# Kernel tuning notes

Hardware: AMD Instinct MI355X
Metric: run time of the kernel (lower is better)

## Reference

```python
import jax, jax.numpy as jnp
import numpy as np
from jax import lax

IN_CH = 256
FILTERS_PER_CH = 2            # expansion = 1 -> 2 filters per input channel
INTER_CH = IN_CH * FILTERS_PER_CH
BUTTERFLY_SIZE = 8
BUTTERFLIES = INTER_CH // 2 // BUTTERFLY_SIZE  # 32
WING = BUTTERFLY_SIZE // 2                      # 4


def setup_inputs() -> dict:
    key = jax.random.key(0)
    k1, k2 = jax.random.split(key)
    x = jax.random.normal(k1, (32, IN_CH, 56, 56), dtype=jnp.float32)
    # depthwise conv weight, PyTorch OIHW with groups=IN_CH: (INTER_CH, 1, 3, 3)
    w = jax.random.normal(k2, (INTER_CH, 1, 3, 3), dtype=jnp.float32) * 0.1
    return {"x": x, "w": w}


def reference(x, w):
    # grouped (depthwise, channel multiplier 2) conv, stride 1, pad 1, no bias
    y = lax.conv_general_dilated(
        x, w,
        window_strides=(1, 1),
        padding=[(1, 1), (1, 1)],
        feature_group_count=IN_CH,
        dimension_numbers=("NCHW", "OIHW", "NCHW"),
    )  # (B, INTER_CH, H, W); channels group-major: 2i,2i+1 from input i
    B, C2, H, W = y.shape
    # extract_sequences: consecutive channels alternate between the two outputs
    y = y.reshape(B, C2 // 2, 2, H, W)
    x1 = y[:, :, 0]  # (B, IN_CH, H, W)
    x2 = y[:, :, 1]
    # swap_wings: within each butterfly, swap the two wings
    s = x2.reshape(B, BUTTERFLIES, 2, WING, H, W)
    x2 = jnp.flip(s, axis=2).reshape(B, C2 // 2, H, W)
    return x1 + x2
```

## Files before the change

### kernel.cpp

```cpp
#include <hip/hip_runtime.h>

#define IN_CH 256
#define IMG_H 56
#define IMG_W 56

typedef float v4f __attribute__((ext_vector_type(4)));

__global__ __launch_bounds__(256) void dwconv_butterfly(
    const float* __restrict__ x, const float* __restrict__ wgt,
    float* __restrict__ out)
{
    const int tid = threadIdx.x;
    const int s   = tid >> 4;
    const int i   = tid & 15;
    const bool active = (s < 14) && (i < 14);

    const int p  = blockIdx.x;
    const int b  = blockIdx.y;
    const int c0 = ((p >> 2) << 3) | (p & 3);
    const int c1 = c0 ^ 4;

    const size_t chan = (size_t)IMG_H * IMG_W;
    const float* x0 = x + ((size_t)b * IN_CH + c0) * chan;
    const float* x1 = x + ((size_t)b * IN_CH + c1) * chan;
    float* o0 = out + ((size_t)b * IN_CH + c0) * chan;
    float* o1 = out + ((size_t)b * IN_CH + c1) * chan;

    float wa[9], wb[9], wc[9], wd[9];
    {
        const float* pa = wgt + (size_t)(2 * c0) * 9;
        const float* pb = wgt + (size_t)(2 * c1 + 1) * 9;
        const float* pc = wgt + (size_t)(2 * c1) * 9;
        const float* pd = wgt + (size_t)(2 * c0 + 1) * 9;
#pragma unroll
        for (int k = 0; k < 9; ++k) {
            wa[k] = pa[k]; wb[k] = pb[k]; wc[k] = pc[k]; wd[k] = pd[k];
        }
    }

    const int row0 = 4 * s - 1;
    const int col  = 4 * i;

    float4 v0[6], v1[6];
#pragma unroll
    for (int k = 0; k < 6; ++k) {
        const int  rr = row0 + k;
        const bool ok = active && (rr >= 0) && (rr < IMG_H);
        if (ok) {
            v0[k] = *(const float4*)(x0 + rr * IMG_W + col);
            v1[k] = *(const float4*)(x1 + rr * IMG_W + col);
        } else {
            v0[k] = make_float4(0.f, 0.f, 0.f, 0.f);
            v1[k] = make_float4(0.f, 0.f, 0.f, 0.f);
        }
    }

    float l0[6], r0h[6], l1[6], r1h[6];
#pragma unroll
    for (int k = 0; k < 6; ++k) {
        const float a = __shfl_up(v0[k].w, 1);
        const float bb = __shfl_up(v1[k].w, 1);
        const float c = __shfl_down(v0[k].x, 1);
        const float d = __shfl_down(v1[k].x, 1);
        l0[k]  = (i == 0)  ? 0.f : a;
        l1[k]  = (i == 0)  ? 0.f : bb;
        r0h[k] = (i == 13) ? 0.f : c;
        r1h[k] = (i == 13) ? 0.f : d;
    }

#pragma unroll
    for (int m = 0; m < 4; ++m) {
        float acc0[4] = {0.f, 0.f, 0.f, 0.f};
        float acc1[4] = {0.f, 0.f, 0.f, 0.f};
#pragma unroll
        for (int kh = 0; kh < 3; ++kh) {
            const int k = m + kh;
            const float e0[6] = {l0[k], v0[k].x, v0[k].y, v0[k].z, v0[k].w, r0h[k]};
            const float e1[6] = {l1[k], v1[k].x, v1[k].y, v1[k].z, v1[k].w, r1h[k]};
#pragma unroll
            for (int kw = 0; kw < 3; ++kw) {
                const float fa = wa[kh * 3 + kw], fb = wb[kh * 3 + kw];
                const float fc = wc[kh * 3 + kw], fd = wd[kh * 3 + kw];
#pragma unroll
                for (int q = 0; q < 4; ++q) {
                    acc0[q] += e0[q + kw] * fa + e1[q + kw] * fb;
                    acc1[q] += e1[q + kw] * fc + e0[q + kw] * fd;
                }
            }
        }
        if (active) {
            const int orow = 4 * s + m;
            v4f s0 = {acc0[0], acc0[1], acc0[2], acc0[3]};
            v4f s1 = {acc1[0], acc1[1], acc1[2], acc1[3]};
            __builtin_nontemporal_store(s0, (v4f*)(o0 + orow * IMG_W + col));
            __builtin_nontemporal_store(s1, (v4f*)(o1 + orow * IMG_W + col));
        }
    }
}

extern "C" void kernel_launch(void* const* d_in, const int* in_sizes, int n_in,
                              void* d_out, int out_size, void* d_ws, size_t ws_size,
                              hipStream_t stream) {
    const float* x = (const float*)d_in[0];
    const float* w = (const float*)d_in[1];
    float* out = (float*)d_out;

    dim3 grid(IN_CH / 2, 32);
    dim3 block(256);
    dwconv_butterfly<<<grid, block, 0, stream>>>(x, w, out);
}
```

Baseline: 190.4 us.

## Process four batches per block with double-buffered register loads

Each block now handles four batch images, striding through the batch with two register buffers so the next tile's global loads are issued before the current tile is computed. Out-of-range rows and lanes are clamped so loads become unconditional, and padding rows are zeroed with selects instead. Nontemporal stores become plain stores and launch bounds request 4 blocks per SM. The aim is to hide memory latency and amortize weight loads, at the cost of higher register pressure and a grid 4x smaller.

```diff
diff --git a/kernel.cpp b/kernel.cpp
--- a/kernel.cpp
+++ b/kernel.cpp
@@ -3,10 +3,13 @@
 #define IN_CH 256
 #define IMG_H 56
 #define IMG_W 56
+#define NBATCH 32
+#define BPG 4
+#define GY (NBATCH / BPG)
 
 typedef float v4f __attribute__((ext_vector_type(4)));
 
-__global__ __launch_bounds__(256) void dwconv_butterfly(
+__global__ __launch_bounds__(256, 4) void dwconv_butterfly(
     const float* __restrict__ x, const float* __restrict__ wgt,
     float* __restrict__ out)
 {
@@ -14,88 +17,115 @@
     const int s   = tid >> 4;
     const int i   = tid & 15;
     const bool active = (s < 14) && (i < 14);
+    const int ss  = (s < 14) ? s : 13;
+    const int ii  = (i < 14) ? i : 13;
 
     const int p  = blockIdx.x;
-    const int b  = blockIdx.y;
+    const int g  = blockIdx.y;
     const int c0 = ((p >> 2) << 3) | (p & 3);
     const int c1 = c0 ^ 4;
 
     const size_t chan = (size_t)IMG_H * IMG_W;
-    const float* x0 = x + ((size_t)b * IN_CH + c0) * chan;
-    const float* x1 = x + ((size_t)b * IN_CH + c1) * chan;
-    float* o0 = out + ((size_t)b * IN_CH + c0) * chan;
-    float* o1 = out + ((size_t)b * IN_CH + c1) * chan;
 
     float wa[9], wb[9], wc[9], wd[9];
     {
         const float* pa = wgt + (size_t)(2 * c0) * 9;
         const float* pb = wgt + (size_t)(2 * c1 + 1) * 9;
         const float* pc = wgt + (size_t)(2 * c1) * 9;
-        const float* pd = wgt + (size_t)(2 * c0 + 1) * 9;
+        const float* pd = wgt + (size_t)(2 * c0) * 9 + 9;
 #pragma unroll
         for (int k = 0; k < 9; ++k) {
             wa[k] = pa[k]; wb[k] = pb[k]; wc[k] = pc[k]; wd[k] = pd[k];
         }
     }
 
-    const int row0 = 4 * s - 1;
-    const int col  = 4 * i;
+    const int row0 = 4 * ss - 1;
+    const int col  = 4 * ii;
 
-    float4 v0[6], v1[6];
+    int  roff[6];
+    bool zrow[6];
 #pragma unroll
     for (int k = 0; k < 6; ++k) {
-        const int  rr = row0 + k;
-        const bool ok = active && (rr >= 0) && (rr < IMG_H);
-        if (ok) {
-            v0[k] = *(const float4*)(x0 + rr * IMG_W + col);
-            v1[k] = *(const float4*)(x1 + rr * IMG_W + col);
-        } else {
-            v0[k] = make_float4(0.f, 0.f, 0.f, 0.f);
-            v1[k] = make_float4(0.f, 0.f, 0.f, 0.f);
-        }
+        const int rr = row0 + k;
+        zrow[k] = (rr < 0) || (rr >= IMG_H);
+        const int rc = rr < 0 ? 0 : (rr >= IMG_H ? IMG_H - 1 : rr);
+        roff[k] = rc * IMG_W + col;
     }
 
-    float l0[6], r0h[6], l1[6], r1h[6];
+    auto load_tile = [&](int b, float4* v0, float4* v1) {
+        const float* x0 = x + ((size_t)b * IN_CH + c0) * chan;
+        const float* x1 = x + ((size_t)b * IN_CH + c1) * chan;
 #pragma unroll
-    for (int k = 0; k < 6; ++k) {
-        const float a = __shfl_up(v0[k].w, 1);
-        const float bb = __shfl_up(v1[k].w, 1);
-        const float c = __shfl_down(v0[k].x, 1);
-        const float d = __shfl_down(v1[k].x, 1);
-        l0[k]  = (i == 0)  ? 0.f : a;
-        l1[k]  = (i == 0)  ? 0.f : bb;
-        r0h[k] = (i == 13) ? 0.f : c;
-        r1h[k] = (i == 13) ? 0.f : d;
-    }
+        for (int k = 0; k < 6; ++k) {
+            v0[k] = *(const float4*)(x0 + roff[k]);
+            v1[k] = *(const float4*)(x1 + roff[k]);
+        }
+    };
+
+    auto compute_tile = [&](int b, const float4* v0, const float4* v1) {
+        float l0[6], r0h[6], l1[6], r1h[6];
+#pragma unroll
+        for (int k = 0; k < 6; ++k) {
+            const float a  = __shfl_up(v0[k].w, 1);
+            const float bb = __shfl_up(v1[k].w, 1);
+            const float c  = __shfl_down(v0[k].x, 1);
+            const float d  = __shfl_down(v1[k].x, 1);
+            l0[k]  = (i == 0)  ? 0.f : a;
+            l1[k]  = (i == 0)  ? 0.f : bb;
+            r0h[k] = (i == 13) ? 0.f : c;
+            r1h[k] = (i == 13) ? 0.f : d;
+        }
+
+        float* o0 = out + ((size_t)b * IN_CH + c0) * chan;
+        float* o1 = out + ((size_t)b * IN_CH + c1) * chan;
 
 #pragma unroll
-    for (int m = 0; m < 4; ++m) {
-        float acc0[4] = {0.f, 0.f, 0.f, 0.f};
-        float acc1[4] = {0.f, 0.f, 0.f, 0.f};
+        for (int m = 0; m < 4; ++m) {
+            float acc0[4] = {0.f, 0.f, 0.f, 0.f};
+            float acc1[4] = {0.f, 0.f, 0.f, 0.f};
 #pragma unroll
-        for (int kh = 0; kh < 3; ++kh) {
-            const int k = m + kh;
-            const float e0[6] = {l0[k], v0[k].x, v0[k].y, v0[k].z, v0[k].w, r0h[k]};
-            const float e1[6] = {l1[k], v1[k].x, v1[k].y, v1[k].z, v1[k].w, r1h[k]};
+            for (int kh = 0; kh < 3; ++kh) {
+                const int k = m + kh;
+                const float z = zrow[k] ? 0.f : 1.f;
+                const float e0[6] = {zrow[k] ? 0.f : l0[k],
+                                     zrow[k] ? 0.f : v0[k].x, zrow[k] ? 0.f : v0[k].y,
+                                     zrow[k] ? 0.f : v0[k].z, zrow[k] ? 0.f : v0[k].w,
+                                     zrow[k] ? 0.f : r0h[k]};
+                const float e1[6] = {zrow[k] ? 0.f : l1[k],
+                                     zrow[k] ? 0.f : v1[k].x, zrow[k] ? 0.f : v1[k].y,
+                                     zrow[k] ? 0.f : v1[k].z, zrow[k] ? 0.f : v1[k].w,
+                                     zrow[k] ? 0.f : r1h[k]};
+                (void)z;
 #pragma unroll
-            for (int kw = 0; kw < 3; ++kw) {
-                const float fa = wa[kh * 3 + kw], fb = wb[kh * 3 + kw];
-                const float fc = wc[kh * 3 + kw], fd = wd[kh * 3 + kw];
+                for (int kw = 0; kw < 3; ++kw) {
+                    const float fa = wa[kh * 3 + kw], fb = wb[kh * 3 + kw];
+                    const float fc = wc[kh * 3 + kw], fd = wd[kh * 3 + kw];
 #pragma unroll
-                for (int q = 0; q < 4; ++q) {
-                    acc0[q] += e0[q + kw] * fa + e1[q + kw] * fb;
-                    acc1[q] += e1[q + kw] * fc + e0[q + kw] * fd;
+                    for (int q = 0; q < 4; ++q) {
+                        acc0[q] += e0[q + kw] * fa + e1[q + kw] * fb;
+                        acc1[q] += e1[q + kw] * fc + e0[q + kw] * fd;
+                    }
                 }
             }
+            if (active) {
+                const int orow = 4 * s + m;
+                *(float4*)(o0 + orow * IMG_W + col) =
+                    make_float4(acc0[0], acc0[1], acc0[2], acc0[3]);
+                *(float4*)(o1 + orow * IMG_W + col) =
+                    make_float4(acc1[0], acc1[1], acc1[2], acc1[3]);
+            }
         }
-        if (active) {
-            const int orow = 4 * s + m;
-            v4f s0 = {acc0[0], acc0[1], acc0[2], acc0[3]};
-            v4f s1 = {acc1[0], acc1[1], acc1[2], acc1[3]};
-            __builtin_nontemporal_store(s0, (v4f*)(o0 + orow * IMG_W + col));
-            __builtin_nontemporal_store(s1, (v4f*)(o1 + orow * IMG_W + col));
-        }
-    }
+    };
+
+    float4 A0[6], A1[6], B0[6], B1[6];
+    load_tile(g,          A0, A1);
+    load_tile(g + GY,     B0, B1);
+    compute_tile(g,          A0, A1);
+    load_tile(g + 2 * GY, A0, A1);
+    compute_tile(g + GY,     B0, B1);
+    load_tile(g + 3 * GY, B0, B1);
+    compute_tile(g + 2 * GY, A0, A1);
+    compute_tile(g + 3 * GY, B0, B1);
 }
 
 extern "C" void kernel_launch(void* const* d_in, const int* in_sizes, int n_in,
@@ -105,7 +135,7 @@
     const float* w = (const float*)d_in[1];
     float* out = (float*)d_out;
 
-    dim3 grid(IN_CH / 2, 32);
+    dim3 grid(IN_CH / 2, GY);
     dim3 block(256);
     dwconv_butterfly<<<grid, block, 0, stream>>>(x, w, out);
 }
```

After: 249.1 us. 30.8% more time.
